# Performance work log

Hardware: AMD Instinct MI355X
Metric: run time of the kernel (lower is better)

Reference implementation:

```python
import jax, jax.numpy as jnp
import numpy as np

D_IN = 512
D_OUT = 512
EPS = 1e-5


def setup_inputs() -> dict:
    key = jax.random.key(0)
    ks = jax.random.split(key, 6)
    B, T = 256, D_OUT + 1  # T includes CLS token (dropped in forward)
    x = jax.random.normal(ks[0], (B, T, D_IN), dtype=jnp.float32)
    s = 1.0 / np.sqrt(D_IN)
    W1 = jax.random.uniform(ks[1], (D_IN, D_IN), jnp.float32, -s, s)
    b1 = jax.random.uniform(ks[2], (D_IN,), jnp.float32, -s, s)
    gamma = jnp.ones((D_IN,), jnp.float32)
    beta = jnp.zeros((D_IN,), jnp.float32)
    Wout = jax.random.uniform(ks[3], (D_OUT, D_IN), jnp.float32, -s, s)  # stacked per-column Linear(d_in,1) weights
    bout = jax.random.uniform(ks[4], (D_OUT,), jnp.float32, -s, s)
    return {"x": x, "W1": W1, "b1": b1, "gamma": gamma, "beta": beta,
            "Wout": Wout, "bout": bout}


def reference(x, W1, b1, gamma, beta, Wout, bout):
    h = x[:, :-1]                              # drop CLS: [B, d_out, d_in]
    h = jnp.einsum('btd,ed->bte', h, W1) + b1  # linear1
    mu = jnp.mean(h, axis=-1, keepdims=True)
    var = jnp.mean(jnp.square(h - mu), axis=-1, keepdims=True)
    h = (h - mu) * jax.lax.rsqrt(var + EPS) * gamma + beta  # LayerNorm
    h = jax.nn.relu(h)
    # per-column head: out[:, t] = h[:, t] @ Wout[t] + bout[t]
    out = jnp.einsum('btd,td->bt', h, Wout) + bout  # [B, d_out]
    return out
```

## Files before the change

kernel.cpp:

```cpp
#include <hip/hip_runtime.h>


#define DIN     512
#define BK      32
#define MT      64
#define THREADS 512
#define NCHUNK  (DIN / BK)
#define ASTR    40
#define BSTR    32

typedef __attribute__((ext_vector_type(8))) short bf16x8;
typedef __attribute__((ext_vector_type(4))) float f32x4;

__device__ __forceinline__ short f2bf(float f) {
    unsigned u = __float_as_uint(f);
    u = u + 0x7fffu + ((u >> 16) & 1u);
    return (short)(u >> 16);
}

__device__ __forceinline__ void gload_lds16(const void* g, void* l) {
    __builtin_amdgcn_global_load_lds(
        (const __attribute__((address_space(1))) unsigned int*)g,
        (__attribute__((address_space(3))) unsigned int*)l,
        16, 0, 0);
}

__global__ void cvt_w1_kernel(const float* __restrict__ w, short* __restrict__ o) {
    int i = blockIdx.x * blockDim.x + threadIdx.x;
    float4 v = ((const float4*)w)[i];
    short4 s;
    s.x = f2bf(v.x); s.y = f2bf(v.y); s.z = f2bf(v.z); s.w = f2bf(v.w);
    ((short4*)o)[i] = s;
}

template<bool WS>
__global__ __launch_bounds__(THREADS, 2)
void fused_head_kernel(const float* __restrict__ x,
                       const float* __restrict__ W1f,
                       const short* __restrict__ W1h,
                       const float* __restrict__ b1,
                       const float* __restrict__ gamma,
                       const float* __restrict__ beta,
                       const float* __restrict__ Wout,
                       const float* __restrict__ bout,
                       float* __restrict__ out) {
    __shared__ __align__(16) short As[MT * ASTR];
    __shared__ __align__(16) short Bs[DIN * BSTR];
    __shared__ float redS[MT][4];
    __shared__ float redQ[MT][4];
    __shared__ float meanA[MT];
    __shared__ float rstdA[MT];

    const int tid  = threadIdx.x;
    const int w    = tid >> 6;
    const int lane = tid & 63;
    const int q    = lane >> 4;
    const int l15  = lane & 15;
    const int rg   = w >> 2;
    const int cg   = w & 3;

    const int m0 = blockIdx.x * MT;
    const int bb = m0 >> 9;
    const int t0 = m0 & 511;
    const float* xbase = x + (size_t)(bb * 513 + t0) * DIN;

    const int ar = tid >> 3;
    const int ak = (tid & 7) * 4;

    const short* bG = W1h + (size_t)(w * 64 + (lane >> 2)) * DIN + (lane & 3) * 8;
    short* bL = Bs + (w * 64) * BSTR;

    f32x4 acc[2][8];
#pragma unroll
    for (int i = 0; i < 2; ++i)
#pragma unroll
        for (int j = 0; j < 8; ++j)
            acc[i][j] = (f32x4){0.f, 0.f, 0.f, 0.f};

    float4 aReg = *(const float4*)(xbase + ar * DIN + ak);

    for (int c = 0; c < NCHUNK; ++c) {
        __syncthreads();
        {
            short4 a4;
            a4.x = f2bf(aReg.x); a4.y = f2bf(aReg.y);
            a4.z = f2bf(aReg.z); a4.w = f2bf(aReg.w);
            *(short4*)(&As[ar * ASTR + ak]) = a4;
        }
        if (WS) {
#pragma unroll
            for (int j = 0; j < 4; ++j)
                gload_lds16(bG + (size_t)(j * 16) * DIN + c * BK,
                            bL + j * 16 * BSTR);
        } else {
            const float* src = W1f + (size_t)tid * DIN + c * BK;
#pragma unroll
            for (int p = 0; p < 8; ++p) {
                float4 v = *(const float4*)(src + p * 4);
                short4 s4;
                s4.x = f2bf(v.x); s4.y = f2bf(v.y);
                s4.z = f2bf(v.z); s4.w = f2bf(v.w);
                *(short4*)(&Bs[tid * BSTR + p * 4]) = s4;
            }
        }
        __syncthreads();

        if (c + 1 < NCHUNK)
            aReg = *(const float4*)(xbase + ar * DIN + (c + 1) * BK + ak);

        bf16x8 af[2], bfr[8];
        const short* Ap = As + (rg * 32 + l15) * ASTR + q * 8;
        af[0] = *(const bf16x8*)Ap;
        af[1] = *(const bf16x8*)(Ap + 16 * ASTR);
        const short* Bp = Bs + (cg * 128 + l15) * BSTR + q * 8;
#pragma unroll
        for (int tj = 0; tj < 8; ++tj)
            bfr[tj] = *(const bf16x8*)(Bp + tj * 16 * BSTR);
#pragma unroll
        for (int ti = 0; ti < 2; ++ti)
#pragma unroll
            for (int tj = 0; tj < 8; ++tj)
                acc[ti][tj] = __builtin_amdgcn_mfma_f32_16x16x32_bf16(
                    af[ti], bfr[tj], acc[ti][tj], 0, 0, 0);
    }

    float b1v[8], gv[8], bv[8];
    const int cb = cg * 128 + l15;
#pragma unroll
    for (int tj = 0; tj < 8; ++tj) {
        int col = cb + tj * 16;
        b1v[tj] = b1[col];
        gv[tj]  = gamma[col];
        bv[tj]  = beta[col];
    }

#pragma unroll
    for (int ti = 0; ti < 2; ++ti)
#pragma unroll
        for (int r = 0; r < 4; ++r) {
            int row = rg * 32 + ti * 16 + q * 4 + r;
            float s = 0.f, s2 = 0.f;
#pragma unroll
            for (int tj = 0; tj < 8; ++tj) {
                float v = acc[ti][tj][r] + b1v[tj];
                s += v; s2 += v * v;
            }
#pragma unroll
            for (int m = 1; m < 16; m <<= 1) {
                s  += __shfl_xor(s,  m, 64);
                s2 += __shfl_xor(s2, m, 64);
            }
            if (l15 == 0) { redS[row][cg] = s; redQ[row][cg] = s2; }
        }
    __syncthreads();
    if (tid < MT) {
        float s  = redS[tid][0] + redS[tid][1] + redS[tid][2] + redS[tid][3];
        float s2 = redQ[tid][0] + redQ[tid][1] + redQ[tid][2] + redQ[tid][3];
        float mean = s * (1.f / DIN);
        float var  = s2 * (1.f / DIN) - mean * mean;
        meanA[tid] = mean;
        rstdA[tid] = rsqrtf(fmaxf(var, 0.f) + 1e-5f);
    }
    __syncthreads();

#pragma unroll
    for (int ti = 0; ti < 2; ++ti)
#pragma unroll
        for (int r = 0; r < 4; ++r) {
            int row = rg * 32 + ti * 16 + q * 4 + r;
            float mean = meanA[row], rs = rstdA[row];
            const float* wrow = Wout + (size_t)(t0 + row) * DIN + cb;
            float s = 0.f;
#pragma unroll
            for (int tj = 0; tj < 8; ++tj) {
                float v = acc[ti][tj][r] + b1v[tj];
                v = (v - mean) * rs * gv[tj] + bv[tj];
                v = fmaxf(v, 0.f);
                s += v * wrow[tj * 16];
            }
#pragma unroll
            for (int m = 1; m < 16; m <<= 1)
                s += __shfl_xor(s, m, 64);
            if (l15 == 0) redS[row][cg] = s;
        }
    __syncthreads();
    if (tid < MT)
        out[m0 + tid] = redS[tid][0] + redS[tid][1] + redS[tid][2] + redS[tid][3]
                        + bout[t0 + tid];
}

extern "C" void kernel_launch(void* const* d_in, const int* in_sizes, int n_in,
                              void* d_out, int out_size, void* d_ws, size_t ws_size,
                              hipStream_t stream) {
    const float* x     = (const float*)d_in[0];
    const float* W1    = (const float*)d_in[1];
    const float* b1    = (const float*)d_in[2];
    const float* gamma = (const float*)d_in[3];
    const float* beta  = (const float*)d_in[4];
    const float* Wout  = (const float*)d_in[5];
    const float* bout  = (const float*)d_in[6];
    float* out = (float*)d_out;

    const int M = 256 * 512;
    dim3 grid(M / MT), block(THREADS);

    if (ws_size >= (size_t)(DIN * DIN) * sizeof(short)) {
        short* W1h = (short*)d_ws;
        cvt_w1_kernel<<<DIN * DIN / (256 * 4), 256, 0, stream>>>(W1, W1h);
        fused_head_kernel<true><<<grid, block, 0, stream>>>(
            x, W1, W1h, b1, gamma, beta, Wout, bout, out);
    } else {
        fused_head_kernel<false><<<grid, block, 0, stream>>>(
            x, W1, nullptr, b1, gamma, beta, Wout, bout, out);
    }
}
```

Measured before the change: 433.1 us.

## Double-buffer A/B LDS tiles, swizzle B layout, and raise occupancy bound

Converts the K-loop to double-buffered LDS stages so the next chunk's W1 tile (via global_load_lds) and the converted x tile are written while MFMAs run on the current buffers, leaving one barrier per iteration instead of two. The B tile moves to a banded, permuted layout meant to avoid LDS bank conflicts for the 16-byte fragment reads. B fragments are loaded in two halves of four to reduce register pressure, and launch bounds go from 2 to 4 blocks per CU. LDS use roughly doubles to about 75 KB per block, which may cap the achievable occupancy below the requested bound.

```diff
diff --git a/kernel.cpp b/kernel.cpp
--- a/kernel.cpp
+++ b/kernel.cpp
@@ -7,7 +7,9 @@
 #define THREADS 512
 #define NCHUNK  (DIN / BK)
 #define ASTR    40
-#define BSTR    32
+#define AS_SZ   (MT * ASTR)
+#define BS_SZ   (DIN * BK)
+#define BANDS   (BK * 16)
 
 typedef __attribute__((ext_vector_type(8))) short bf16x8;
 typedef __attribute__((ext_vector_type(4))) float f32x4;
@@ -33,8 +35,27 @@
     ((short4*)o)[i] = s;
 }
 
+__device__ __forceinline__ void stage_b_fallback(short* dstBuf, const float* W1f,
+                                                 int c, int tid) {
+    const float* src = W1f + (size_t)tid * DIN + c * BK;
+    const int band = tid >> 4, rr = tid & 15;
+    short* dstband = dstBuf + band * BANDS;
+#pragma unroll
+    for (int p = 0; p < 4; ++p) {
+        float4 v0 = *(const float4*)(src + p * 8);
+        float4 v1 = *(const float4*)(src + p * 8 + 4);
+        int P = (rr & 7) + 8 * p + ((rr >> 3) << 5);
+        short* d = dstband + P * 8;
+        short4 s0, s1;
+        s0.x = f2bf(v0.x); s0.y = f2bf(v0.y); s0.z = f2bf(v0.z); s0.w = f2bf(v0.w);
+        s1.x = f2bf(v1.x); s1.y = f2bf(v1.y); s1.z = f2bf(v1.z); s1.w = f2bf(v1.w);
+        *(short4*)d = s0;
+        *(short4*)(d + 4) = s1;
+    }
+}
+
 template<bool WS>
-__global__ __launch_bounds__(THREADS, 2)
+__global__ __launch_bounds__(THREADS, 4)
 void fused_head_kernel(const float* __restrict__ x,
                        const float* __restrict__ W1f,
                        const short* __restrict__ W1h,
@@ -44,8 +65,8 @@
                        const float* __restrict__ Wout,
                        const float* __restrict__ bout,
                        float* __restrict__ out) {
-    __shared__ __align__(16) short As[MT * ASTR];
-    __shared__ __align__(16) short Bs[DIN * BSTR];
+    __shared__ __align__(16) short As[2][AS_SZ];
+    __shared__ __align__(16) short Bs[2][BS_SZ];
     __shared__ float redS[MT][4];
     __shared__ float redQ[MT][4];
     __shared__ float meanA[MT];
@@ -67,8 +88,12 @@
     const int ar = tid >> 3;
     const int ak = (tid & 7) * 4;
 
-    const short* bG = W1h + (size_t)(w * 64 + (lane >> 2)) * DIN + (lane & 3) * 8;
-    short* bL = Bs + (w * 64) * BSTR;
+    const int brow = (lane & 7) + ((lane >> 5) << 3);
+    const int bq   = (lane >> 3) & 3;
+    const short* bG = W1h + (size_t)(w * 64 + brow) * DIN + bq * 8;
+
+    const int bOff = cg * (8 * BANDS)
+                   + ((l15 & 7) + 8 * q + ((l15 >> 3) << 5)) * 8;
 
     f32x4 acc[2][8];
 #pragma unroll
@@ -78,50 +103,74 @@
             acc[i][j] = (f32x4){0.f, 0.f, 0.f, 0.f};
 
     float4 aReg = *(const float4*)(xbase + ar * DIN + ak);
+    if (WS) {
+#pragma unroll
+        for (int j = 0; j < 4; ++j)
+            gload_lds16(bG + (size_t)(j * 16) * DIN,
+                        &Bs[0][w * (4 * BANDS) + j * BANDS]);
+    } else {
+        stage_b_fallback(Bs[0], W1f, 0, tid);
+    }
+    {
+        short4 a4;
+        a4.x = f2bf(aReg.x); a4.y = f2bf(aReg.y);
+        a4.z = f2bf(aReg.z); a4.w = f2bf(aReg.w);
+        *(short4*)(&As[0][ar * ASTR + ak]) = a4;
+    }
+    aReg = *(const float4*)(xbase + ar * DIN + BK + ak);
+    __syncthreads();
 
     for (int c = 0; c < NCHUNK; ++c) {
-        __syncthreads();
-        {
+        const int cur = c & 1, nxt = cur ^ 1;
+
+        if (c + 1 < NCHUNK) {
+            if (WS) {
+#pragma unroll
+                for (int j = 0; j < 4; ++j)
+                    gload_lds16(bG + (size_t)(j * 16) * DIN + (c + 1) * BK,
+                                &Bs[nxt][w * (4 * BANDS) + j * BANDS]);
+            } else {
+                stage_b_fallback(Bs[nxt], W1f, c + 1, tid);
+            }
             short4 a4;
             a4.x = f2bf(aReg.x); a4.y = f2bf(aReg.y);
             a4.z = f2bf(aReg.z); a4.w = f2bf(aReg.w);
-            *(short4*)(&As[ar * ASTR + ak]) = a4;
-        }
-        if (WS) {
-#pragma unroll
-            for (int j = 0; j < 4; ++j)
-                gload_lds16(bG + (size_t)(j * 16) * DIN + c * BK,
-                            bL + j * 16 * BSTR);
-        } else {
-            const float* src = W1f + (size_t)tid * DIN + c * BK;
-#pragma unroll
-            for (int p = 0; p < 8; ++p) {
-                float4 v = *(const float4*)(src + p * 4);
-                short4 s4;
-                s4.x = f2bf(v.x); s4.y = f2bf(v.y);
-                s4.z = f2bf(v.z); s4.w = f2bf(v.w);
-                *(short4*)(&Bs[tid * BSTR + p * 4]) = s4;
+            *(short4*)(&As[nxt][ar * ASTR + ak]) = a4;
+        }
+        if (c + 2 < NCHUNK)
+            aReg = *(const float4*)(xbase + ar * DIN + (c + 2) * BK + ak);
+
+        const short* Ap = &As[cur][(rg * 32 + l15) * ASTR + q * 8];
+        bf16x8 af0 = *(const bf16x8*)Ap;
+        bf16x8 af1 = *(const bf16x8*)(Ap + 16 * ASTR);
+        const short* Bp = &Bs[cur][bOff];
+        {
+            bf16x8 bfr[4];
+#pragma unroll
+            for (int tj = 0; tj < 4; ++tj)
+                bfr[tj] = *(const bf16x8*)(Bp + tj * BANDS);
+#pragma unroll
+            for (int tj = 0; tj < 4; ++tj) {
+                acc[0][tj] = __builtin_amdgcn_mfma_f32_16x16x32_bf16(
+                    af0, bfr[tj], acc[0][tj], 0, 0, 0);
+                acc[1][tj] = __builtin_amdgcn_mfma_f32_16x16x32_bf16(
+                    af1, bfr[tj], acc[1][tj], 0, 0, 0);
+            }
+        }
+        {
+            bf16x8 bfr[4];
+#pragma unroll
+            for (int tj = 0; tj < 4; ++tj)
+                bfr[tj] = *(const bf16x8*)(Bp + (tj + 4) * BANDS);
+#pragma unroll
+            for (int tj = 0; tj < 4; ++tj) {
+                acc[0][tj + 4] = __builtin_amdgcn_mfma_f32_16x16x32_bf16(
+                    af0, bfr[tj], acc[0][tj + 4], 0, 0, 0);
+                acc[1][tj + 4] = __builtin_amdgcn_mfma_f32_16x16x32_bf16(
+                    af1, bfr[tj], acc[1][tj + 4], 0, 0, 0);
             }
         }
         __syncthreads();
-
-        if (c + 1 < NCHUNK)
-            aReg = *(const float4*)(xbase + ar * DIN + (c + 1) * BK + ak);
-
-        bf16x8 af[2], bfr[8];
-        const short* Ap = As + (rg * 32 + l15) * ASTR + q * 8;
-        af[0] = *(const bf16x8*)Ap;
-        af[1] = *(const bf16x8*)(Ap + 16 * ASTR);
-        const short* Bp = Bs + (cg * 128 + l15) * BSTR + q * 8;
-#pragma unroll
-        for (int tj = 0; tj < 8; ++tj)
-            bfr[tj] = *(const bf16x8*)(Bp + tj * 16 * BSTR);
-#pragma unroll
-        for (int ti = 0; ti < 2; ++ti)
-#pragma unroll
-            for (int tj = 0; tj < 8; ++tj)
-                acc[ti][tj] = __builtin_amdgcn_mfma_f32_16x16x32_bf16(
-                    af[ti], bfr[tj], acc[ti][tj], 0, 0, 0);
     }
 
     float b1v[8], gv[8], bv[8];
```

Result: slower. 475.7 us (+9.8%).
